# Optimization experiments

Hardware: AMD Instinct MI355X
Metric: run time of the kernel (lower is better)

## Reference

```python
import jax, jax.numpy as jnp
import numpy as np

# LIF constants from norse.LIFParameters in the module
DT = 1e-3
TAU_MEM_INV = 4.0      # 1 / tau_mem, tau_mem = 0.25
TAU_SYN_INV = 200.0    # norse default 1/5e-3
V_TH = 0.1
ALPHA = 50.0           # super-spike surrogate slope
NHEAD = 4

@jax.custom_vjp
def spike(x):
    # SuperSpike: heaviside forward, surrogate gradient backward
    return (x > 0).astype(x.dtype)

def _spike_fwd(x):
    return spike(x), x

def _spike_bwd(x, g):
    return (g / (ALPHA * jnp.abs(x) + 1.0) ** 2,)

spike.defvjp(_spike_fwd, _spike_bwd)

def lif_reservoir(x, Win, Wres):
    # x: [B,S,I] -> spikes z: [B,S,R]. All batches start from zero state,
    # so the per-batch python loop of the original vectorizes over B.
    inp = jnp.einsum('bsi,ir->bsr', x, Win)  # precompute input currents
    B, S, R = inp.shape

    def step(carry, cur):  # cur: [B,R]
        v, i, z = carry
        total = cur + z @ Wres  # z=0 at t=0, matching the t>0 branch
        v_dec = v + DT * TAU_MEM_INV * (-v + i)  # v_leak = 0
        i_dec = i * (1.0 - DT * TAU_SYN_INV)
        z_new = spike(v_dec - V_TH)
        v_new = (1.0 - z_new) * v_dec            # v_reset = 0
        i_new = i_dec + total
        return (v_new, i_new, z_new), z_new

    init = (jnp.zeros((B, R), x.dtype),) * 3
    _, zs = jax.lax.scan(step, init, jnp.swapaxes(inp, 0, 1))
    return jnp.swapaxes(zs, 0, 1)  # [B,S,R]

def layer_norm(x, g, b, eps=1e-5):
    m = x.mean(-1, keepdims=True)
    v = ((x - m) ** 2).mean(-1, keepdims=True)
    return (x - m) / jnp.sqrt(v + eps) * g + b

def encoder_layer(x, Wqkv, bqkv, Wo, bo, g1, b1, g2, b2, W1, c1, W2, c2):
    # Post-norm TransformerEncoderLayer, relu activation, dropout=eval(0)
    B, S, D = x.shape
    dh = D // NHEAD
    qkv = x @ Wqkv.T + bqkv
    q, k, v = jnp.split(qkv, 3, axis=-1)
    rh = lambda t: t.reshape(B, S, NHEAD, dh)
    q, k, v = rh(q), rh(k), rh(v)
    scores = jnp.einsum('bqhd,bkhd->bhqk', q, k) / jnp.sqrt(jnp.asarray(dh, x.dtype))
    attn = jax.nn.softmax(scores, axis=-1)
    o = jnp.einsum('bhqk,bkhd->bqhd', attn, v).reshape(B, S, D)
    o = o @ Wo.T + bo
    x = layer_norm(x + o, g1, b1)
    ff = jax.nn.relu(x @ W1.T + c1) @ W2.T + c2
    return layer_norm(x + ff, g2, b2)

def setup_inputs() -> dict:
    key = jax.random.key(0)
    B, S, I, R, D, L, FF = 32, 1024, 8, 512, 256, 2, 1024
    ks = jax.random.split(key, 16)
    x = jax.random.normal(ks[0], (B, S, I), jnp.float32)
    Win = jax.random.normal(ks[1], (I, R), jnp.float32) * 0.1
    # sparse reservoir: density 0.2, values uniform [0,1)
    mask = (jax.random.uniform(ks[2], (R, R)) < 0.2).astype(jnp.float32)
    Wres = jax.random.uniform(ks[3], (R, R), jnp.float32) * mask
    Wread = jax.random.normal(ks[4], (D, R), jnp.float32) * 0.04
    bread = jnp.zeros((D,), jnp.float32)
    Wqkv = jax.random.normal(ks[5], (L, 3 * D, D), jnp.float32) * 0.05
    bqkv = jnp.zeros((L, 3 * D), jnp.float32)
    Wo = jax.random.normal(ks[6], (L, D, D), jnp.float32) * 0.05
    bo = jnp.zeros((L, D), jnp.float32)
    ln1_g = jnp.ones((L, D), jnp.float32)
    ln1_b = jnp.zeros((L, D), jnp.float32)
    ln2_g = jnp.ones((L, D), jnp.float32)
    ln2_b = jnp.zeros((L, D), jnp.float32)
    Wff1 = jax.random.normal(ks[7], (L, FF, D), jnp.float32) * 0.05
    bff1 = jnp.zeros((L, FF), jnp.float32)
    Wff2 = jax.random.normal(ks[8], (L, D, FF), jnp.float32) * 0.05
    bff2 = jnp.zeros((L, D), jnp.float32)
    return dict(x=x, Win=Win, Wres=Wres, Wread=Wread, bread=bread,
                Wqkv=Wqkv, bqkv=bqkv, Wo=Wo, bo=bo,
                ln1_g=ln1_g, ln1_b=ln1_b, ln2_g=ln2_g, ln2_b=ln2_b,
                Wff1=Wff1, bff1=bff1, Wff2=Wff2, bff2=bff2)

def reference(x, Win, Wres, Wread, bread, Wqkv, bqkv, Wo, bo,
              ln1_g, ln1_b, ln2_g, ln2_b, Wff1, bff1, Wff2, bff2):
    z = lif_reservoir(x, Win, Wres)          # [B,S,R] spike trains
    h = z @ Wread.T + bread                  # readout to transformer_dim
    for l in range(Wqkv.shape[0]):           # fixed small num_layers
        h = encoder_layer(h, Wqkv[l], bqkv[l], Wo[l], bo[l],
                          ln1_g[l], ln1_b[l], ln2_g[l], ln2_b[l],
                          Wff1[l], bff1[l], Wff2[l], bff2[l])
    return h
```

## Files before the change

### kernel.cpp

```cpp
#include <hip/hip_runtime.h>
#include <stdint.h>

using short8  = __attribute__((ext_vector_type(8))) short;
using floatx4 = __attribute__((ext_vector_type(4))) float;

typedef unsigned short u16;
typedef unsigned int u32;
typedef unsigned long long u64;

#define AS1(p) ((const __attribute__((address_space(1))) void*)(p))
#define AS3(p) ((__attribute__((address_space(3))) void*)(p))

__device__ __forceinline__ float bs2f(u16 u) { return __uint_as_float(((u32)u) << 16); }
__device__ __forceinline__ u16 f2bs(float f) {
  u32 x = __float_as_uint(f);
  x += 0x7FFFu + ((x >> 16) & 1u);
  return (u16)(x >> 16);
}
__device__ __forceinline__ float lo16(u32 u) { return __uint_as_float(u << 16); }
__device__ __forceinline__ float hi16(u32 u) { return __uint_as_float(u & 0xFFFF0000u); }

__global__ __launch_bounds__(256) void cvt_all_k(
    const float* __restrict__ s0, const float* __restrict__ s1,
    const float* __restrict__ s2, const float* __restrict__ s3,
    const float* __restrict__ s4, u16* __restrict__ d0, u16* __restrict__ d1,
    u16* __restrict__ d2, u16* __restrict__ d3, u16* __restrict__ d4) {
  const int i = blockIdx.x * 256 + threadIdx.x;
  if (i < 131072)        d0[i] = f2bs(s0[i]);
  else if (i < 524288)   d1[i - 131072] = f2bs(s1[i - 131072]);
  else if (i < 655360)   d2[i - 524288] = f2bs(s2[i - 524288]);
  else if (i < 1179648)  d3[i - 655360] = f2bs(s3[i - 655360]);
  else                   d4[i - 1179648] = f2bs(s4[i - 1179648]);
}

__global__ __launch_bounds__(512) void inp_k(const float* __restrict__ x,
                                             const float* __restrict__ Win,
                                             float* __restrict__ inp) {
  const int row = blockIdx.x;
  const int r = threadIdx.x;
  const float* xr = x + (size_t)row * 8;
  float s = 0.f;
#pragma unroll
  for (int k = 0; k < 8; ++k) s = fmaf(Win[k * 512 + r], xr[k], s);
  inp[(size_t)row * 512 + r] = s;
}

__global__ __launch_bounds__(64, 1) void reservoir_k(
    const float* __restrict__ inp,
    const float* __restrict__ Wres,
    u16* __restrict__ zout)
{
  const int b = blockIdx.x;
  const int c = threadIdx.x & 63;
  const float* ib = inp + (size_t)b * 524288 + c * 8;
  u16* zb = zout + (size_t)b * 524288 + c * 8;
  float v[8] = {}, ci[8] = {}, rec[8] = {};
  u32 pz = 0;
  for (int tb = 0; tb < 128; ++tb) {
    float4 xa[8], xc[8];
#pragma unroll
    for (int u = 0; u < 8; ++u) {
      const float* p = ib + (size_t)(tb * 8 + u) * 512;
      xa[u] = *(const float4*)p;
      xc[u] = *(const float4*)(p + 4);
    }
    asm volatile("" ::: "memory");
    float sv[8], sci[8];
#pragma unroll
    for (int j = 0; j < 8; ++j) { sv[j] = v[j]; sci[j] = ci[j]; }
    const u32 spz = pz;
    u32 togg = 0;
#pragma unroll
    for (int u = 0; u < 8; ++u) {
      const int t = tb * 8 + u;
      const float in[8] = {xa[u].x, xa[u].y, xa[u].z, xa[u].w,
                           xc[u].x, xc[u].y, xc[u].z, xc[u].w};
      u32 nzb = 0;
      u32 zw[4];
#pragma unroll
      for (int j = 0; j < 8; ++j) {
        const float vdec = __fadd_rn(v[j], __fmul_rn(0.004f, __fadd_rn(-v[j], ci[j])));
        const int zc = (__fadd_rn(vdec, -0.1f) > 0.f) ? 1 : 0;
        v[j] = zc ? 0.f : vdec;
        nzb |= (u32)zc << j;
        ci[j] = __fadd_rn(__fmul_rn(ci[j], 0.8f), __fadd_rn(in[j], rec[j]));
        if (j & 1) zw[j >> 1] |= zc ? 0x3F800000u : 0u;
        else       zw[j >> 1]  = zc ? 0x3F80u : 0u;
      }
      *(uint4*)(zb + (size_t)t * 512) = make_uint4(zw[0], zw[1], zw[2], zw[3]);
      togg |= nzb ^ pz;
      pz = nzb;
    }
    const u64 anyt = __ballot(togg != 0);
    if (anyt) {
#pragma unroll
      for (int j = 0; j < 8; ++j) { v[j] = sv[j]; ci[j] = sci[j]; }
      pz = spz;
#pragma unroll 1
      for (int u = 0; u < 8; ++u) {
        const int t = tb * 8 + u;
        const float in[8] = {xa[u].x, xa[u].y, xa[u].z, xa[u].w,
                             xc[u].x, xc[u].y, xc[u].z, xc[u].w};
        u32 nzb = 0;
        u32 zw[4];
#pragma unroll
        for (int j = 0; j < 8; ++j) {
          const float vdec = __fadd_rn(v[j], __fmul_rn(0.004f, __fadd_rn(-v[j], ci[j])));
          const int zc = (__fadd_rn(vdec, -0.1f) > 0.f) ? 1 : 0;
          v[j] = zc ? 0.f : vdec;
          nzb |= (u32)zc << j;
          ci[j] = __fadd_rn(__fmul_rn(ci[j], 0.8f), __fadd_rn(in[j], rec[j]));
          if (j & 1) zw[j >> 1] |= zc ? 0x3F800000u : 0u;
          else       zw[j >> 1]  = zc ? 0x3F80u : 0u;
        }
        *(uint4*)(zb + (size_t)t * 512) = make_uint4(zw[0], zw[1], zw[2], zw[3]);
        const u64 a2 = __ballot((nzb ^ pz) != 0);
        if (a2) {
#pragma unroll
          for (int j = 0; j < 8; ++j) {
            const u64 nm = __ballot((nzb >> j) & 1);
            const u64 pm = __ballot((pz >> j) & 1);
            u64 on   = nm & ~pm;
            u64 offm = pm & ~nm;
            while (on) {
              const int cc = __builtin_ctzll(on); on &= on - 1;
              const float* wr = Wres + ((size_t)(cc * 8 + j) << 9) + c * 8;
              const float4 w0 = *(const float4*)wr;
              const float4 w1 = *(const float4*)(wr + 4);
              rec[0] += w0.x; rec[1] += w0.y; rec[2] += w0.z; rec[3] += w0.w;
              rec[4] += w1.x; rec[5] += w1.y; rec[6] += w1.z; rec[7] += w1.w;
            }
            while (offm) {
              const int cc = __builtin_ctzll(offm); offm &= offm - 1;
              const float* wr = Wres + ((size_t)(cc * 8 + j) << 9) + c * 8;
              const float4 w0 = *(const float4*)wr;
              const float4 w1 = *(const float4*)(wr + 4);
              rec[0] -= w0.x; rec[1] -= w0.y; rec[2] -= w0.z; rec[3] -= w0.w;
              rec[4] -= w1.x; rec[5] -= w1.y; rec[6] -= w1.z; rec[7] -= w1.w;
            }
          }
        }
        pz = nzb;
      }
    }
  }
}

enum { MODE_BF16 = 0, MODE_F32 = 1, MODE_DUAL = 2, MODE_QKV = 3 };

template <int WM, int WN, int MODE>
__global__ __launch_bounds__(WM * WN * 64) void gemm_bt(
    const u16* __restrict__ A, const u16* __restrict__ B,
    const float* __restrict__ bias, void* __restrict__ C0,
    void* __restrict__ C1, void* __restrict__ C2, int K, int lda, int ldb,
    int ldc, long long sA, long long sB, long long sC, float scale, int relu)
{
  constexpr int BM = WM * 64, BN = WN * 64, BK = 32;
  constexpr int NT = WM * WN * 64;
  constexpr int CA = BM * 4 / NT, CB = BN * 4 / NT;
  __shared__ __align__(16) u16 As[BM * BK];
  __shared__ __align__(16) u16 Bs[BN * BK];
  const int tid = threadIdx.x;
  const int bz = blockIdx.z;
  const u16* Ab = A + (size_t)bz * sA + (size_t)blockIdx.y * BM * lda;
  const u16* Bb = B + (size_t)bz * sB + (size_t)blockIdx.x * BN * ldb;
  const int wavei = tid >> 6, lane = tid & 63;
  const int r16 = lane & 15, quad = lane >> 4;
  const int wm = (wavei % WM) * 64, wn = (wavei / WM) * 64;
  floatx4 acc[4][4] = {};
  for (int k0 = 0; k0 < K; k0 += BK) {
#pragma unroll
    for (int c = 0; c < CA; ++c) {
      const int idx = c * NT + tid;
      const int row = idx >> 2, kc = (idx & 3) << 3;
      __builtin_amdgcn_global_load_lds(AS1(Ab + (size_t)row * lda + k0 + kc),
                                       AS3(As + idx * 8), 16, 0, 0);
    }
#pragma unroll
    for (int c = 0; c < CB; ++c) {
      const int idx = c * NT + tid;
      const int row = idx >> 2, kc = (idx & 3) << 3;
      __builtin_amdgcn_global_load_lds(AS1(Bb + (size_t)row * ldb + k0 + kc),
                                       AS3(Bs + idx * 8), 16, 0, 0);
    }
    __syncthreads();
    short8 af[4], bfr[4];
#pragma unroll
    for (int i = 0; i < 4; ++i)
      af[i] = *(const short8*)&As[(wm + i * 16 + r16) * BK + quad * 8];
#pragma unroll
    for (int i = 0; i < 4; ++i)
      bfr[i] = *(const short8*)&Bs[(wn + i * 16 + r16) * BK + quad * 8];
#pragma unroll
    for (int i = 0; i < 4; ++i)
#pragma unroll
      for (int j = 0; j < 4; ++j)
        acc[i][j] = __builtin_amdgcn_mfma_f32_16x16x32_bf16(af[i], bfr[j], acc[i][j], 0, 0, 0);
    __syncthreads();
  }
#pragma unroll
  for (int i = 0; i < 4; ++i) {
#pragma unroll
    for (int j = 0; j < 4; ++j) {
#pragma unroll
      for (int q = 0; q < 4; ++q) {
        const int m = blockIdx.y * BM + wm + i * 16 + quad * 4 + q;
        const int n = blockIdx.x * BN + wn + j * 16 + r16;
        float val = acc[i][j][q] * scale;
        if (bias) val += bias[n];
        if (relu) val = fmaxf(val, 0.f);
        if constexpr (MODE == MODE_BF16) {
          ((u16*)C0)[(size_t)bz * sC + (size_t)m * ldc + n] = f2bs(val);
        } else if constexpr (MODE == MODE_F32) {
          ((float*)C0)[(size_t)m * ldc + n] = val;
        } else if constexpr (MODE == MODE_DUAL) {
          ((float*)C0)[(size_t)m * ldc + n] = val;
          ((u16*)C1)[(size_t)m * ldc + n] = f2bs(val);
        } else if constexpr (MODE == MODE_QKV) {
          const int b = m >> 10, s = m & 1023;
          const u16 outv = f2bs(val);
          const int h = (n & 255) >> 6, d = n & 63;
          if (n < 256)
            ((u16*)C0)[(((size_t)(b * 4 + h)) * 1024 + s) * 64 + d] = outv;
          else if (n < 512)
            ((u16*)C1)[(((size_t)(b * 4 + h)) * 1024 + s) * 64 + d] = outv;
          else
            ((u16*)C2)[(((size_t)(b * 4 + h)) * 64 + d) * 1024 + s] = outv;
        }
      }
    }
  }
}

__global__ __launch_bounds__(256) void attn_k(
    const u16* __restrict__ q_s,
    const u16* __restrict__ k_s,
    const u16* __restrict__ v_t,
    u16* __restrict__ o16)
{
  constexpr int LQ = 72, LV = 136, LP = 136;
  __shared__ __align__(16) u16 Qs[128 * LQ];
  __shared__ __align__(16) u16 Ks[128 * LQ];
  __shared__ __align__(16) u16 Vt[64 * LV];
  __shared__ __align__(16) u16 Ps[128 * LP];
  const int tid = threadIdx.x;
  const int w = tid >> 6, lane = tid & 63;
  const int r16 = lane & 15, quad = lane >> 4;
  const int p = blockIdx.y;
  const int q0 = blockIdx.x * 128;
  const u16* qg = q_s + ((size_t)p * 1024 + q0) * 64;
  const u16* kg = k_s + (size_t)p * 65536;
  const u16* vg = v_t + (size_t)p * 65536;

#pragma unroll
  for (int it = 0; it < 4; ++it) {
    const int idx = it * 256 + tid;
    const int row = idx >> 3, c8 = (idx & 7) * 8;
    *(uint4*)&Qs[row * LQ + c8] = *(const uint4*)(qg + (size_t)row * 64 + c8);
    *(uint4*)&Ks[row * LQ + c8] = *(const uint4*)(kg + (size_t)row * 64 + c8);
  }
#pragma unroll
  for (int it = 0; it < 4; ++it) {
    const int idx = it * 256 + tid;
    const int row = idx >> 4, c8 = (idx & 15) * 8;
    *(uint4*)&Vt[row * LV + c8] = *(const uint4*)(vg + (size_t)row * 1024 + c8);
  }
  __syncthreads();

  short8 aq[2][2];
#pragma unroll
  for (int i = 0; i < 2; ++i)
#pragma unroll
    for (int kc = 0; kc < 2; ++kc)
      aq[i][kc] = *(const short8*)&Qs[(w * 32 + i * 16 + r16) * LQ + kc * 32 + quad * 8];

  floatx4 o[2][4] = {};
  float mr[2][4], l[2][4];
#pragma unroll
  for (int i = 0; i < 2; ++i)
#pragma unroll
    for (int q = 0; q < 4; ++q) { mr[i][q] = -3e38f; l[i][q] = 0.f; }

  for (int kt = 0; kt < 8; ++kt) {
    uint4 kpre[4], vpre[4];
    if (kt < 7) {
      const u16* kgn = kg + (size_t)(kt + 1) * 128 * 64;
#pragma unroll
      for (int it = 0; it < 4; ++it) {
        const int idx = it * 256 + tid;
        kpre[it] = *(const uint4*)(kgn + (size_t)(idx >> 3) * 64 + (idx & 7) * 8);
        vpre[it] = *(const uint4*)(vg + (size_t)(idx >> 4) * 1024 + (kt + 1) * 128 + (idx & 15) * 8);
      }
    }
    floatx4 s[2][8] = {};
#pragma unroll
    for (int kc = 0; kc < 2; ++kc) {
#pragma unroll
      for (int f = 0; f < 8; ++f) {
        const short8 bk = *(const short8*)&Ks[(f * 16 + r16) * LQ + kc * 32 + quad * 8];
#pragma unroll
        for (int i = 0; i < 2; ++i)
          s[i][f] = __builtin_amdgcn_mfma_f32_16x16x32_bf16(aq[i][kc], bk, s[i][f], 0, 0, 0);
      }
    }
#pragma unroll
    for (int i = 0; i < 2; ++i) {
      float mt[4] = {-3e38f, -3e38f, -3e38f, -3e38f};
#pragma unroll
      for (int f = 0; f < 8; ++f)
#pragma unroll
        for (int q = 0; q < 4; ++q) {
          s[i][f][q] *= 0.125f;
          mt[q] = fmaxf(mt[q], s[i][f][q]);
        }
#pragma unroll
      for (int off = 8; off > 0; off >>= 1)
#pragma unroll
        for (int q = 0; q < 4; ++q) mt[q] = fmaxf(mt[q], __shfl_xor(mt[q], off));
      float al[4], rs[4] = {};
#pragma unroll
      for (int q = 0; q < 4; ++q) {
        const float mn = fmaxf(mr[i][q], mt[q]);
        al[q] = __expf(mr[i][q] - mn);
        mr[i][q] = mn;
      }
#pragma unroll
      for (int f = 0; f < 8; ++f)
#pragma unroll
        for (int q = 0; q < 4; ++q) {
          const float pv = __expf(s[i][f][q] - mr[i][q]);
          s[i][f][q] = pv;
          rs[q] += pv;
        }
#pragma unroll
      for (int off = 8; off > 0; off >>= 1)
#pragma unroll
        for (int q = 0; q < 4; ++q) rs[q] += __shfl_xor(rs[q], off);
#pragma unroll
      for (int q = 0; q < 4; ++q) l[i][q] = l[i][q] * al[q] + rs[q];
#pragma unroll
      for (int n = 0; n < 4; ++n)
#pragma unroll
        for (int q = 0; q < 4; ++q) o[i][n][q] *= al[q];
#pragma unroll
      for (int f = 0; f < 8; ++f)
#pragma unroll
        for (int q = 0; q < 4; ++q)
          Ps[(w * 32 + i * 16 + quad * 4 + q) * LP + f * 16 + r16] = f2bs(s[i][f][q]);
    }
#pragma unroll
    for (int kc = 0; kc < 4; ++kc) {
      short8 ap[2];
#pragma unroll
      for (int i = 0; i < 2; ++i)
        ap[i] = *(const short8*)&Ps[(w * 32 + i * 16 + r16) * LP + kc * 32 + quad * 8];
#pragma unroll
      for (int n = 0; n < 4; ++n) {
        const short8 bv = *(const short8*)&Vt[(n * 16 + r16) * LV + kc * 32 + quad * 8];
#pragma unroll
        for (int i = 0; i < 2; ++i)
          o[i][n] = __builtin_amdgcn_mfma_f32_16x16x32_bf16(ap[i], bv, o[i][n], 0, 0, 0);
      }
    }
    __syncthreads();
    if (kt < 7) {
#pragma unroll
      for (int it = 0; it < 4; ++it) {
        const int idx = it * 256 + tid;
        *(uint4*)&Ks[(idx >> 3) * LQ + (idx & 7) * 8] = kpre[it];
        *(uint4*)&Vt[(idx >> 4) * LV + (idx & 15) * 8] = vpre[it];
      }
      __syncthreads();
    }
  }
  const int bb = p >> 2, hh = p & 3;
#pragma unroll
  for (int i = 0; i < 2; ++i)
#pragma unroll
    for (int q = 0; q < 4; ++q) {
      const float inv = 1.f / l[i][q];
      const int srow = q0 + w * 32 + i * 16 + quad * 4 + q;
#pragma unroll
      for (int n = 0; n < 4; ++n)
        o16[((size_t)bb * 1024 + srow) * 256 + hh * 64 + n * 16 + r16] =
            f2bs(o[i][n][q] * inv);
    }
}

__global__ __launch_bounds__(256) void ln_k(const float* __restrict__ x,
                                            const float* __restrict__ add,
                                            const float* __restrict__ g,
                                            const float* __restrict__ bta,
                                            float* __restrict__ y32,
                                            u16* __restrict__ y16) {
  const int row = blockIdx.x * 4 + (threadIdx.x >> 6);
  const int lane = threadIdx.x & 63;
  const size_t base = (size_t)row * 256 + lane * 4;
  const float4 xv = *(const float4*)(x + base);
  const float4 av = *(const float4*)(add + base);
  float sv[4] = {xv.x + av.x, xv.y + av.y, xv.z + av.z, xv.w + av.w};
  float sum = sv[0] + sv[1] + sv[2] + sv[3];
#pragma unroll
  for (int off = 32; off > 0; off >>= 1) sum += __shfl_xor(sum, off);
  const float mean = sum * (1.f / 256.f);
  float var = 0.f;
  float d[4];
#pragma unroll
  for (int i = 0; i < 4; ++i) { d[i] = sv[i] - mean; var += d[i] * d[i]; }
#pragma unroll
  for (int off = 32; off > 0; off >>= 1) var += __shfl_xor(var, off);
  var *= (1.f / 256.f);
  const float inv = 1.f / sqrtf(var + 1e-5f);
  float yv[4];
#pragma unroll
  for (int i = 0; i < 4; ++i)
    yv[i] = d[i] * inv * g[lane * 4 + i] + bta[lane * 4 + i];
  if (y32) *(float4*)(y32 + base) = make_float4(yv[0], yv[1], yv[2], yv[3]);
  if (y16) {
    const u32 p0 = (u32)f2bs(yv[0]) | ((u32)f2bs(yv[1]) << 16);
    const u32 p1 = (u32)f2bs(yv[2]) | ((u32)f2bs(yv[3]) << 16);
    *(uint2*)(y16 + base) = make_uint2(p0, p1);
  }
}

extern "C" void kernel_launch(void* const* d_in, const int* in_sizes, int n_in,
                              void* d_out, int out_size, void* d_ws,
                              size_t ws_size, hipStream_t stream) {
  (void)in_sizes; (void)n_in; (void)out_size; (void)ws_size;
  const float* x     = (const float*)d_in[0];
  const float* Win   = (const float*)d_in[1];
  const float* Wres  = (const float*)d_in[2];
  const float* Wread = (const float*)d_in[3];
  const float* bread = (const float*)d_in[4];
  const float* Wqkv  = (const float*)d_in[5];
  const float* bqkv  = (const float*)d_in[6];
  const float* Wo    = (const float*)d_in[7];
  const float* bo    = (const float*)d_in[8];
  const float* g1    = (const float*)d_in[9];
  const float* b1    = (const float*)d_in[10];
  const float* g2    = (const float*)d_in[11];
  const float* b2    = (const float*)d_in[12];
  const float* W1    = (const float*)d_in[13];
  const float* c1    = (const float*)d_in[14];
  const float* W2    = (const float*)d_in[15];
  const float* c2    = (const float*)d_in[16];

  char* ws = (char*)d_ws;
  size_t off = 0;
  auto carve = [&](size_t bytes) {
    char* p = ws + off;
    off += (bytes + 255) & ~(size_t)255;
    return p;
  };
  u16* z      = (u16*)carve((size_t)32 * 1024 * 512 * 2);
  u16* wrd16  = (u16*)carve((size_t)256 * 512 * 2);
  u16* wqkv16 = (u16*)carve((size_t)2 * 768 * 256 * 2);
  u16* wo16   = (u16*)carve((size_t)2 * 256 * 256 * 2);
  u16* w116   = (u16*)carve((size_t)2 * 1024 * 256 * 2);
  u16* w216   = (u16*)carve((size_t)2 * 256 * 1024 * 2);
  u16* q_s    = (u16*)carve((size_t)128 * 1024 * 64 * 2);
  u16* k_s    = (u16*)carve((size_t)128 * 1024 * 64 * 2);
  u16* v_t    = (u16*)carve((size_t)128 * 64 * 1024 * 2);
  float* h32  = (float*)carve((size_t)32768 * 256 * 4);
  float* lin  = (float*)carve((size_t)32768 * 256 * 4);
  u16* h16    = (u16*)carve((size_t)32768 * 256 * 2);
  u16* ff1    = (u16*)carve((size_t)32768 * 1024 * 2);
  u16* o16    = h16;
  float* inp  = (float*)ff1;

  cvt_all_k<<<dim3(6656), dim3(256), 0, stream>>>(Wread, Wqkv, Wo, W1, W2,
                                                  wrd16, wqkv16, wo16, w116,
                                                  w216);
  inp_k<<<dim3(32768), dim3(512), 0, stream>>>(x, Win, inp);
  reservoir_k<<<dim3(32), dim3(64), 0, stream>>>(inp, Wres, z);

  gemm_bt<2, 2, MODE_DUAL><<<dim3(2, 256, 1), dim3(256), 0, stream>>>(
      z, wrd16, bread, h32, h16, nullptr, 512, 512, 512, 256, 0, 0, 0, 1.0f, 0);

  for (int l = 0; l < 2; ++l) {
    gemm_bt<2, 2, MODE_QKV><<<dim3(6, 256, 1), dim3(256), 0, stream>>>(
        h16, wqkv16 + (size_t)l * 196608, bqkv + l * 768, q_s, k_s, v_t, 256,
        256, 256, 0, 0, 0, 0, 1.0f, 0);
    attn_k<<<dim3(8, 128), dim3(256), 0, stream>>>(q_s, k_s, v_t, o16);
    gemm_bt<2, 2, MODE_F32><<<dim3(2, 256, 1), dim3(256), 0, stream>>>(
        o16, wo16 + (size_t)l * 65536, bo + l * 256, lin, nullptr, nullptr,
        256, 256, 256, 256, 0, 0, 0, 1.0f, 0);
    ln_k<<<dim3(8192), dim3(256), 0, stream>>>(h32, lin, g1 + l * 256,
                                               b1 + l * 256, h32, h16);
    gemm_bt<2, 2, MODE_BF16><<<dim3(8, 256, 1), dim3(256), 0, stream>>>(
        h16, w116 + (size_t)l * 262144, c1 + l * 1024, ff1, nullptr, nullptr,
        256, 256, 256, 1024, 0, 0, 0, 1.0f, 1);
    gemm_bt<2, 2, MODE_F32><<<dim3(2, 256, 1), dim3(256), 0, stream>>>(
        ff1, w216 + (size_t)l * 262144, c2 + l * 256, lin, nullptr, nullptr,
        1024, 1024, 1024, 256, 0, 0, 0, 1.0f, 0);
    float* y32 = (l == 1) ? (float*)d_out : h32;
    u16* y16 = (l == 1) ? nullptr : h16;
    ln_k<<<dim3(8192), dim3(256), 0, stream>>>(h32, lin, g2 + l * 256,
                                               b2 + l * 256, y32, y16);
  }
}
```

Measured before the change: 1.460 ms.

## Double-buffer reservoir input through LDS and drop speculative replay path

The input projection now writes currents in a permuted layout, split into two 256-float halves, so each 8-step chunk is contiguous. The reservoir kernel streams each chunk into a double-buffered LDS tile with async global-to-LDS loads issued two chunks ahead, so global load latency overlaps with the serial time-step loop. The old speculative path, which ran 8 steps and replayed them when any spike toggled, is replaced by a single pass that updates the recurrent term at every step where a toggle occurs. This avoids redundant recomputation but adds a ballot and branch on every step, plus manual waitcnt encodings that must stay correct.

```diff
diff --git a/kernel.cpp b/kernel.cpp
--- a/kernel.cpp
+++ b/kernel.cpp
@@ -42,7 +42,9 @@
   float s = 0.f;
 #pragma unroll
   for (int k = 0; k < 8; ++k) s = fmaf(Win[k * 512 + r], xr[k], s);
-  inp[(size_t)row * 512 + r] = s;
+  const int c = r >> 3, j = r & 7;
+  const int idx = (j < 4) ? (c * 4 + j) : (256 + c * 4 + (j - 4));
+  inp[(size_t)row * 512 + idx] = s;
 }
 
 __global__ __launch_bounds__(64, 1) void reservoir_k(
@@ -52,29 +54,30 @@
 {
   const int b = blockIdx.x;
   const int c = threadIdx.x & 63;
-  const float* ib = inp + (size_t)b * 524288 + c * 8;
+  __shared__ __align__(16) float s_in[2][4096];
+  const float* ib = inp + (size_t)b * 524288;
   u16* zb = zout + (size_t)b * 524288 + c * 8;
   float v[8] = {}, ci[8] = {}, rec[8] = {};
   u32 pz = 0;
-  for (int tb = 0; tb < 128; ++tb) {
-    float4 xa[8], xc[8];
+#pragma unroll
+  for (int i = 0; i < 16; ++i)
+    __builtin_amdgcn_global_load_lds(AS1(ib + i * 256 + c * 4),
+                                     AS3(&s_in[0][i * 256 + c * 4]), 16, 0, 0);
+#pragma unroll
+  for (int i = 0; i < 16; ++i)
+    __builtin_amdgcn_global_load_lds(AS1(ib + 4096 + i * 256 + c * 4),
+                                     AS3(&s_in[1][i * 256 + c * 4]), 16, 0, 0);
+  for (int g = 0; g < 128; ++g) {
+    const int buf = g & 1;
+    if (g < 126) __builtin_amdgcn_s_waitcnt(0x4F70);
+    else         __builtin_amdgcn_s_waitcnt(0x0F70);
+    asm volatile("" ::: "memory");
 #pragma unroll
     for (int u = 0; u < 8; ++u) {
-      const float* p = ib + (size_t)(tb * 8 + u) * 512;
-      xa[u] = *(const float4*)p;
-      xc[u] = *(const float4*)(p + 4);
-    }
-    asm volatile("" ::: "memory");
-    float sv[8], sci[8];
-#pragma unroll
-    for (int j = 0; j < 8; ++j) { sv[j] = v[j]; sci[j] = ci[j]; }
-    const u32 spz = pz;
-    u32 togg = 0;
-#pragma unroll
-    for (int u = 0; u < 8; ++u) {
-      const int t = tb * 8 + u;
-      const float in[8] = {xa[u].x, xa[u].y, xa[u].z, xa[u].w,
-                           xc[u].x, xc[u].y, xc[u].z, xc[u].w};
+      const int t = g * 8 + u;
+      const float4 xa = *(const float4*)&s_in[buf][u * 512 + c * 4];
+      const float4 xc = *(const float4*)&s_in[buf][u * 512 + 256 + c * 4];
+      const float in[8] = {xa.x, xa.y, xa.z, xa.w, xc.x, xc.y, xc.z, xc.w};
       u32 nzb = 0;
       u32 zw[4];
 #pragma unroll
@@ -88,60 +91,41 @@
         else       zw[j >> 1]  = zc ? 0x3F80u : 0u;
       }
       *(uint4*)(zb + (size_t)t * 512) = make_uint4(zw[0], zw[1], zw[2], zw[3]);
-      togg |= nzb ^ pz;
-      pz = nzb;
-    }
-    const u64 anyt = __ballot(togg != 0);
-    if (anyt) {
-#pragma unroll
-      for (int j = 0; j < 8; ++j) { v[j] = sv[j]; ci[j] = sci[j]; }
-      pz = spz;
-#pragma unroll 1
-      for (int u = 0; u < 8; ++u) {
-        const int t = tb * 8 + u;
-        const float in[8] = {xa[u].x, xa[u].y, xa[u].z, xa[u].w,
-                             xc[u].x, xc[u].y, xc[u].z, xc[u].w};
-        u32 nzb = 0;
-        u32 zw[4];
+      const u64 anyt = __ballot((nzb ^ pz) != 0);
+      if (anyt) {
 #pragma unroll
         for (int j = 0; j < 8; ++j) {
-          const float vdec = __fadd_rn(v[j], __fmul_rn(0.004f, __fadd_rn(-v[j], ci[j])));
-          const int zc = (__fadd_rn(vdec, -0.1f) > 0.f) ? 1 : 0;
-          v[j] = zc ? 0.f : vdec;
-          nzb |= (u32)zc << j;
-          ci[j] = __fadd_rn(__fmul_rn(ci[j], 0.8f), __fadd_rn(in[j], rec[j]));
-          if (j & 1) zw[j >> 1] |= zc ? 0x3F800000u : 0u;
-          else       zw[j >> 1]  = zc ? 0x3F80u : 0u;
-        }
-        *(uint4*)(zb + (size_t)t * 512) = make_uint4(zw[0], zw[1], zw[2], zw[3]);
-        const u64 a2 = __ballot((nzb ^ pz) != 0);
-        if (a2) {
-#pragma unroll
-          for (int j = 0; j < 8; ++j) {
-            const u64 nm = __ballot((nzb >> j) & 1);
-            const u64 pm = __ballot((pz >> j) & 1);
-            u64 on   = nm & ~pm;
-            u64 offm = pm & ~nm;
-            while (on) {
-              const int cc = __builtin_ctzll(on); on &= on - 1;
-              const float* wr = Wres + ((size_t)(cc * 8 + j) << 9) + c * 8;
-              const float4 w0 = *(const float4*)wr;
-              const float4 w1 = *(const float4*)(wr + 4);
-              rec[0] += w0.x; rec[1] += w0.y; rec[2] += w0.z; rec[3] += w0.w;
-              rec[4] += w1.x; rec[5] += w1.y; rec[6] += w1.z; rec[7] += w1.w;
-            }
-            while (offm) {
-              const int cc = __builtin_ctzll(offm); offm &= offm - 1;
-              const float* wr = Wres + ((size_t)(cc * 8 + j) << 9) + c * 8;
-              const float4 w0 = *(const float4*)wr;
-              const float4 w1 = *(const float4*)(wr + 4);
-              rec[0] -= w0.x; rec[1] -= w0.y; rec[2] -= w0.z; rec[3] -= w0.w;
-              rec[4] -= w1.x; rec[5] -= w1.y; rec[6] -= w1.z; rec[7] -= w1.w;
-            }
+          const u64 nm = __ballot((nzb >> j) & 1);
+          const u64 pm = __ballot((pz >> j) & 1);
+          u64 on   = nm & ~pm;
+          u64 offm = pm & ~nm;
+          while (on) {
+            const int cc = __builtin_ctzll(on); on &= on - 1;
+            const float* wr = Wres + ((size_t)(cc * 8 + j) << 9) + c * 8;
+            const float4 w0 = *(const float4*)wr;
+            const float4 w1 = *(const float4*)(wr + 4);
+            rec[0] += w0.x; rec[1] += w0.y; rec[2] += w0.z; rec[3] += w0.w;
+            rec[4] += w1.x; rec[5] += w1.y; rec[6] += w1.z; rec[7] += w1.w;
+          }
+          while (offm) {
+            const int cc = __builtin_ctzll(offm); offm &= offm - 1;
+            const float* wr = Wres + ((size_t)(cc * 8 + j) << 9) + c * 8;
+            const float4 w0 = *(const float4*)wr;
+            const float4 w1 = *(const float4*)(wr + 4);
+            rec[0] -= w0.x; rec[1] -= w0.y; rec[2] -= w0.z; rec[3] -= w0.w;
+            rec[4] -= w1.x; rec[5] -= w1.y; rec[6] -= w1.z; rec[7] -= w1.w;
           }
         }
-        pz = nzb;
-      }
+      }
+      pz = nzb;
+    }
+    asm volatile("" ::: "memory");
+    if (g + 2 < 128) {
+      const float* gt = ib + (size_t)(g + 2) * 4096;
+#pragma unroll
+      for (int i = 0; i < 16; ++i)
+        __builtin_amdgcn_global_load_lds(AS1(gt + i * 256 + c * 4),
+                                         AS3(&s_in[buf][i * 256 + c * 4]), 16, 0, 0);
     }
   }
 }
```

After: 1.373 ms. 1.06x faster.
